# Kernel tuning notes

Measured on AMD Instinct MI355X. Metric: run time of the kernel, lower is better.

The kernel has to match this reference:

```python
import jax, jax.numpy as jnp
import numpy as np

B, H, W, C = 32, 64, 64, 256
NH, WS, SHIFT = 8, 8, 4
HD = C // NH
N = WS * WS           # tokens per window
NW = (H // WS) * (W // WS)
HID = 4 * C
EPS_LN = 1e-5
LOGIT_MAX = float(np.log(1.0 / 0.01))


def _rel_coords_table():
    ch = np.arange(-(WS - 1), WS, dtype=np.float32)
    t = np.stack(np.meshgrid(ch, ch, indexing='ij'), axis=-1)  # (2WS-1, 2WS-1, 2)
    t = t / (WS - 1) * 8.0
    t = np.sign(t) * np.log2(np.abs(t) + 1.0) / np.log2(8.0)
    return t.reshape(-1, 2)  # ((2WS-1)^2, 2)


def _rel_pos_index():
    coords = np.stack(np.meshgrid(np.arange(WS), np.arange(WS), indexing='ij'))
    cf = coords.reshape(2, -1)
    rel = (cf[:, :, None] - cf[:, None, :]).transpose(1, 2, 0).copy()
    rel[:, :, 0] += WS - 1
    rel[:, :, 1] += WS - 1
    rel[:, :, 0] *= 2 * WS - 1
    return rel.sum(-1)  # (N, N) int


def _attn_mask():
    img = np.zeros((H, W), np.float32)
    cnt = 0
    for hs in (slice(0, -WS), slice(-WS, -SHIFT), slice(-SHIFT, None)):
        for ws in (slice(0, -WS), slice(-WS, -SHIFT), slice(-SHIFT, None)):
            img[hs, ws] = cnt
            cnt += 1
    mw = img.reshape(H // WS, WS, W // WS, WS).transpose(0, 2, 1, 3).reshape(-1, N)
    diff = mw[:, None, :] - mw[:, :, None]
    return np.where(diff != 0, -100.0, 0.0).astype(np.float32)  # (NW, N, N)


_RCT = jnp.asarray(_rel_coords_table())
_RPI = jnp.asarray(_rel_pos_index())
_MASK = jnp.asarray(_attn_mask())


def _ln(x, g, b):
    mu = jnp.mean(x, axis=-1, keepdims=True)
    var = jnp.mean(jnp.square(x - mu), axis=-1, keepdims=True)
    return (x - mu) * jax.lax.rsqrt(var + EPS_LN) * g + b


def _l2n(x):
    return x / jnp.sqrt(jnp.maximum(jnp.sum(x * x, axis=-1, keepdims=True), 1e-12))


def setup_inputs() -> dict:
    key = jax.random.key(0)
    ks = jax.random.split(key, 16)
    s = 0.02
    return {
        'x': jax.random.normal(ks[0], (B, H * W, C), jnp.float32),
        'qkv_w': jax.random.normal(ks[1], (C, 3 * C), jnp.float32) * s,
        'q_bias': jnp.zeros((C,), jnp.float32),
        'v_bias': jnp.zeros((C,), jnp.float32),
        'logit_scale': jnp.full((NH, 1, 1), np.log(10.0), jnp.float32),
        'cpb_w1': jax.random.normal(ks[2], (2, 512), jnp.float32) * s,
        'cpb_b1': jnp.zeros((512,), jnp.float32),
        'cpb_w2': jax.random.normal(ks[3], (512, NH), jnp.float32) * s,
        'proj_w': jax.random.normal(ks[4], (C, C), jnp.float32) * s,
        'proj_b': jnp.zeros((C,), jnp.float32),
        'norm1_g': jnp.ones((C,), jnp.float32),
        'norm1_b': jnp.zeros((C,), jnp.float32),
        'fc1_w': jax.random.normal(ks[5], (C, HID), jnp.float32) * s,
        'fc1_b': jnp.zeros((HID,), jnp.float32),
        'fc2_w': jax.random.normal(ks[6], (HID, C), jnp.float32) * s,
        'fc2_b': jnp.zeros((C,), jnp.float32),
        'norm2_g': jnp.ones((C,), jnp.float32),
        'norm2_b': jnp.zeros((C,), jnp.float32),
    }


def reference(x, qkv_w, q_bias, v_bias, logit_scale, cpb_w1, cpb_b1, cpb_w2,
              proj_w, proj_b, norm1_g, norm1_b, fc1_w, fc1_b, fc2_w, fc2_b,
              norm2_g, norm2_b):
    shortcut = x
    xs = x.reshape(B, H, W, C)
    # cyclic shift
    xs = jnp.roll(xs, shift=(-SHIFT, -SHIFT), axis=(1, 2))
    # window partition -> (B*NW, N, C)
    xw = xs.reshape(B, H // WS, WS, W // WS, WS, C).transpose(0, 1, 3, 2, 4, 5)
    xw = xw.reshape(B * NW, N, C)

    # qkv projection (kernel without bias, then split q/v biases, k bias zero)
    qkv_bias = jnp.concatenate([q_bias, jnp.zeros_like(q_bias), v_bias], axis=0)
    qkv = xw @ qkv_w + qkv_bias
    qkv = qkv.reshape(B * NW, N, 3, NH, HD).transpose(2, 0, 3, 1, 4)
    q, k, v = qkv[0], qkv[1], qkv[2]  # (B*NW, NH, N, HD)

    # cosine attention
    attn = jnp.einsum('bhnd,bhmd->bhnm', _l2n(q), _l2n(k))
    scale = jnp.exp(jnp.minimum(logit_scale, LOGIT_MAX))  # (NH,1,1)
    attn = attn * scale

    # CPB-MLP relative position bias
    table = jax.nn.relu(_RCT @ cpb_w1 + cpb_b1) @ cpb_w2          # ((2WS-1)^2, NH)
    bias = table[_RPI]                                            # (N, N, NH)
    bias = 16.0 * jax.nn.sigmoid(bias.transpose(2, 0, 1))         # (NH, N, N)
    attn = attn + bias[None]

    # shifted-window mask
    attn = attn.reshape(B, NW, NH, N, N) + _MASK[None, :, None]
    attn = jax.nn.softmax(attn.reshape(B * NW, NH, N, N), axis=-1)

    out = jnp.einsum('bhnm,bhmd->bhnd', attn, v)
    out = out.transpose(0, 2, 1, 3).reshape(B * NW, N, C)
    out = out @ proj_w + proj_b

    # window reverse + reverse shift
    out = out.reshape(B, H // WS, W // WS, WS, WS, C).transpose(0, 1, 3, 2, 4, 5)
    out = out.reshape(B, H, W, C)
    out = jnp.roll(out, shift=(SHIFT, SHIFT), axis=(1, 2)).reshape(B, H * W, C)

    # SwinV2 post-norm residuals
    x = shortcut + _ln(out, norm1_g, norm1_b)
    h = jax.nn.gelu(x @ fc1_w + fc1_b, approximate=False) @ fc2_w + fc2_b
    x = x + _ln(h, norm2_g, norm2_b)
    return x
```

## Files before the change

kernel.cpp:

```cpp
#include <hip/hip_runtime.h>


#define TOKS 131072
#define LOGIT_MAX 4.60517018598809136804f

typedef __attribute__((ext_vector_type(8))) short short8;
typedef __attribute__((ext_vector_type(4))) float f32x4;

__device__ __forceinline__ float b2f(unsigned short s) {
    union { unsigned int u; float f; } x; x.u = ((unsigned int)s) << 16; return x.f;
}
__device__ __forceinline__ unsigned short f2b(float f) {
    union { float f; unsigned int u; } x; x.f = f;
    unsigned int r = x.u + 0x7fffu + ((x.u >> 16) & 1u);
    return (unsigned short)(r >> 16);
}

#define MFMA16(a, b, c) __builtin_amdgcn_mfma_f32_16x16x32_bf16((a), (b), (c), 0, 0, 0)

#define GLOAD_LDS16(g, l)                                                      \
    __builtin_amdgcn_global_load_lds(                                          \
        (const __attribute__((address_space(1))) void*)(g),                    \
        (__attribute__((address_space(3))) void*)(l), 16, 0, 0)


__global__ __launch_bounds__(256) void cvt_kernel(const float* __restrict__ in,
                                                  unsigned short* __restrict__ out, int n) {
    int i = (blockIdx.x * 256 + threadIdx.x) * 4;
    if (i >= n) return;
    float4 v = *(const float4*)(in + i);
    ushort4 o;
    o.x = f2b(v.x); o.y = f2b(v.y); o.z = f2b(v.z); o.w = f2b(v.w);
    *(ushort4*)(out + i) = o;
}

__global__ __launch_bounds__(256) void wt_kernel(const float* __restrict__ src,
                                                 unsigned short* __restrict__ dst,
                                                 int K, int N) {
    int idx = blockIdx.x * 256 + threadIdx.x;
    if (idx >= K * N) return;
    int n = idx / K, k = idx - n * K;
    dst[idx] = f2b(src[(size_t)k * N + n]);
}

__device__ __forceinline__ float cpb_coord(int d) {
    float t = (float)d * (8.0f / 7.0f);
    float a = log2f(fabsf(t) + 1.0f) * (1.0f / 3.0f);
    return t < 0.0f ? -a : a;
}

__global__ __launch_bounds__(256) void cpb_kernel(
    const float* __restrict__ w1, const float* __restrict__ b1, const float* __restrict__ w2,
    const float* __restrict__ qb, const float* __restrict__ vb,
    float* __restrict__ biasT, float* __restrict__ qkv_bias)
{
    __shared__ float tbl[225];
    int h = blockIdx.x, t = threadIdx.x;
    if (t < 225) {
        float r0 = cpb_coord(t / 15 - 7), r1 = cpb_coord(t % 15 - 7);
        float acc = 0.f;
        for (int j = 0; j < 512; ++j) {
            float hid = fmaxf(r0 * w1[j] + r1 * w1[512 + j] + b1[j], 0.f);
            acc += hid * w2[j * 8 + h];
        }
        tbl[t] = acc;
    }
    __syncthreads();
    for (int o = t; o < 4096; o += 256) {
        int i = o >> 6, j = o & 63;
        int idx = ((i >> 3) - (j >> 3) + 7) * 15 + ((i & 7) - (j & 7) + 7);
        biasT[h * 4096 + o] = 16.0f / (1.0f + __expf(-tbl[idx]));
    }
    if (h == 0)
        for (int n = t; n < 768; n += 256)
            qkv_bias[n] = n < 256 ? qb[n] : (n < 512 ? 0.f : vb[n - 512]);
}

template<int EPI, int GX>
__global__ __launch_bounds__(256) void gemm_bt(
    const unsigned short* __restrict__ A, const unsigned short* __restrict__ Bt,
    const float* __restrict__ bias, unsigned short* __restrict__ out,
    int M, int N, int K)
{
    __shared__ __align__(16) unsigned short sA[2][128 * 32];
    __shared__ __align__(16) unsigned short sB[2][128 * 32];
    const int tid = threadIdx.x;
    const int lane = tid & 63;
    const int wave = tid >> 6;
    const int wm = (wave >> 1) * 64, wn = (wave & 1) * 64;
    const int nwg = GX * (int)gridDim.y;
    int flat = (int)(blockIdx.y * GX + blockIdx.x);
    flat = (flat & 7) * (nwg >> 3) + (flat >> 3);
    const int bx = flat % GX;
    const int by = flat / GX;
    const int m0 = by * 128, n0 = bx * 128;
    const int l15 = lane & 15, lq = lane >> 4;
    const int r0 = tid >> 2, c0 = (tid & 3) << 3;

    const unsigned short* pA0 = A + (size_t)(m0 + r0) * K + c0;
    const unsigned short* pA1 = A + (size_t)(m0 + r0 + 64) * K + c0;
    const unsigned short* pB0 = Bt + (size_t)(n0 + r0) * K + c0;
    const unsigned short* pB1 = Bt + (size_t)(n0 + r0 + 64) * K + c0;

    auto stage = [&](int buf, int k0) {
        unsigned short* a = &sA[buf][wave * 512];
        unsigned short* b = &sB[buf][wave * 512];
        GLOAD_LDS16(pA0 + k0, a);
        GLOAD_LDS16(pA1 + k0, a + 2048);
        GLOAD_LDS16(pB0 + k0, b);
        GLOAD_LDS16(pB1 + k0, b + 2048);
    };

    f32x4 acc[4][4] = {};
    auto compute = [&](int buf) {
        short8 af[4], bw[4];
        #pragma unroll
        for (int t = 0; t < 4; ++t) {
            af[t] = *(const short8*)&sA[buf][(wm + t * 16 + l15) * 32 + lq * 8];
            bw[t] = *(const short8*)&sB[buf][(wn + t * 16 + l15) * 32 + lq * 8];
        }
        #pragma unroll
        for (int tm = 0; tm < 4; ++tm)
            #pragma unroll
            for (int tn = 0; tn < 4; ++tn)
                acc[tm][tn] = MFMA16(af[tm], bw[tn], acc[tm][tn]);
    };

    const int nt = K >> 5;
    stage(0, 0);
    for (int t = 0; t < nt - 1; ++t) {
        stage((t & 1) ^ 1, (t + 1) << 5);
        asm volatile("s_waitcnt vmcnt(4)" ::: "memory");
        __builtin_amdgcn_s_barrier();
        asm volatile("" ::: "memory");
        compute(t & 1);
        asm volatile("s_waitcnt lgkmcnt(0)" ::: "memory");
        __builtin_amdgcn_s_barrier();
    }
    asm volatile("s_waitcnt vmcnt(0)" ::: "memory");
    __builtin_amdgcn_s_barrier();
    asm volatile("" ::: "memory");
    compute((nt - 1) & 1);

    float bv[4];
    #pragma unroll
    for (int tn = 0; tn < 4; ++tn) bv[tn] = bias[n0 + wn + tn * 16 + l15];

    #pragma unroll
    for (int tm = 0; tm < 4; ++tm)
        #pragma unroll
        for (int tn = 0; tn < 4; ++tn)
            #pragma unroll
            for (int r = 0; r < 4; ++r) {
                int gm = m0 + wm + tm * 16 + lq * 4 + r;
                int gn = n0 + wn + tn * 16 + l15;
                float v = acc[tm][tn][r] + bv[tn];
                if constexpr (EPI == 2) {
                    float e = __expf(v * fmaf(-0.0713548162972754f, v * v,
                                              -1.5957691216057308f));
                    v = v * __builtin_amdgcn_rcpf(1.0f + e);
                }
                if constexpr (EPI == 1) {
                    int s = gn >> 8, hd = gn & 255;
                    out[((size_t)(s * 8 + (hd >> 5)) * TOKS + gm) * 32 + (hd & 31)] = f2b(v);
                } else {
                    out[(size_t)gm * N + gn] = f2b(v);
                }
            }
}

template<int MODE>
__global__ __launch_bounds__(256) void gemm_ln(
    const unsigned short* __restrict__ A, const unsigned short* __restrict__ Bt,
    const float* __restrict__ bias,
    const float* __restrict__ residf, const unsigned short* __restrict__ residb,
    const float* __restrict__ lng, const float* __restrict__ lnb,
    unsigned short* __restrict__ outb, float* __restrict__ outf, int K)
{
    __shared__ __align__(16) unsigned short sA[2][64 * 32];
    __shared__ __align__(16) unsigned short sB[2][256 * 32];
    const int tid = threadIdx.x;
    const int lane = tid & 63;
    const int wave = tid >> 6;
    const int wn = wave * 64;
    const int m0 = blockIdx.x * 64;
    const int l15 = lane & 15, lq = lane >> 4;
    const int r0 = tid >> 2, c0 = (tid & 3) << 3;

    const unsigned short* pA  = A + (size_t)(m0 + r0) * K + c0;
    const unsigned short* pB0 = Bt + (size_t)r0 * K + c0;
    const unsigned short* pB1 = pB0 + (size_t)64 * K;
    const unsigned short* pB2 = pB0 + (size_t)128 * K;
    const unsigned short* pB3 = pB0 + (size_t)192 * K;

    auto stage = [&](int buf, int k0) {
        unsigned short* a = &sA[buf][wave * 512];
        unsigned short* b = &sB[buf][wave * 512];
        GLOAD_LDS16(pA + k0, a);
        GLOAD_LDS16(pB0 + k0, b);
        GLOAD_LDS16(pB1 + k0, b + 2048);
        GLOAD_LDS16(pB2 + k0, b + 4096);
        GLOAD_LDS16(pB3 + k0, b + 6144);
    };

    f32x4 acc[4][4] = {};
    auto compute = [&](int buf) {
        short8 af[4], bw[4];
        #pragma unroll
        for (int t = 0; t < 4; ++t) {
            af[t] = *(const short8*)&sA[buf][(t * 16 + l15) * 32 + lq * 8];
            bw[t] = *(const short8*)&sB[buf][(wn + t * 16 + l15) * 32 + lq * 8];
        }
        #pragma unroll
        for (int tm = 0; tm < 4; ++tm)
            #pragma unroll
            for (int tn = 0; tn < 4; ++tn)
                acc[tm][tn] = MFMA16(af[tm], bw[tn], acc[tm][tn]);
    };

    const int nt = K >> 5;
    stage(0, 0);
    for (int t = 0; t < nt - 1; ++t) {
        stage((t & 1) ^ 1, (t + 1) << 5);
        asm volatile("s_waitcnt vmcnt(5)" ::: "memory");
        __builtin_amdgcn_s_barrier();
        asm volatile("" ::: "memory");
        compute(t & 1);
        asm volatile("s_waitcnt lgkmcnt(0)" ::: "memory");
        __builtin_amdgcn_s_barrier();
    }
    asm volatile("s_waitcnt vmcnt(0)" ::: "memory");
    __builtin_amdgcn_s_barrier();
    asm volatile("" ::: "memory");
    compute((nt - 1) & 1);
    asm volatile("s_waitcnt lgkmcnt(0)" ::: "memory");
    __builtin_amdgcn_s_barrier();

    float bv[4], gv[4], ev[4];
    #pragma unroll
    for (int tn = 0; tn < 4; ++tn) {
        int gn = wn + tn * 16 + l15;
        bv[tn] = bias[gn]; gv[tn] = lng[gn]; ev[tn] = lnb[gn];
    }

    float* sums = (float*)&sA[0][0];
    float* sqs  = (float*)&sA[0][0] + 256;
    #pragma unroll
    for (int tm = 0; tm < 4; ++tm)
        #pragma unroll
        for (int r = 0; r < 4; ++r) {
            int rl = tm * 16 + lq * 4 + r;
            float s = 0.f, q = 0.f;
            #pragma unroll
            for (int tn = 0; tn < 4; ++tn) {
                float v = acc[tm][tn][r] + bv[tn];
                s += v; q += v * v;
            }
            #pragma unroll
            for (int o = 1; o < 16; o <<= 1) { s += __shfl_xor(s, o); q += __shfl_xor(q, o); }
            if (l15 == 0) { sums[rl * 4 + wave] = s; sqs[rl * 4 + wave] = q; }
        }
    __syncthreads();

    #pragma unroll
    for (int tm = 0; tm < 4; ++tm)
        #pragma unroll
        for (int r = 0; r < 4; ++r) {
            int rl = tm * 16 + lq * 4 + r;
            float s = sums[rl * 4] + sums[rl * 4 + 1] + sums[rl * 4 + 2] + sums[rl * 4 + 3];
            float q = sqs[rl * 4] + sqs[rl * 4 + 1] + sqs[rl * 4 + 2] + sqs[rl * 4 + 3];
            float mu = s * (1.0f / 256.0f);
            float rs = rsqrtf(q * (1.0f / 256.0f) - mu * mu + 1e-5f);
            size_t rowo = (size_t)(m0 + rl) * 256;
            #pragma unroll
            for (int tn = 0; tn < 4; ++tn) {
                int gn = wn + tn * 16 + l15;
                float v = acc[tm][tn][r] + bv[tn];
                float nv = (v - mu) * rs * gv[tn] + ev[tn];
                if constexpr (MODE == 1)
                    outb[rowo + gn] = f2b(residf[rowo + gn] + nv);
                else
                    outf[rowo + gn] = b2f(residb[rowo + gn]) + nv;
            }
        }
}


__device__ __forceinline__ int regid(int wy, int wx, int t) {
    int y = wy * 8 + (t >> 3), x = wx * 8 + (t & 7);
    int ry = (y < 56) ? 0 : (y < 60 ? 1 : 2);
    int rx = (x < 56) ? 0 : (x < 60 ? 1 : 2);
    return ry * 3 + rx;
}

__device__ __forceinline__ void load_norm(const unsigned short* __restrict__ p,
                                          unsigned short* __restrict__ dst, int lane) {
    union U { uint4 u; unsigned short s[8]; };
    U ld[4];
    #pragma unroll
    for (int c = 0; c < 4; ++c) ld[c].u = *(const uint4*)(p + c * 8);
    float f[32]; float ss = 0.f;
    #pragma unroll
    for (int c = 0; c < 4; ++c)
        #pragma unroll
        for (int j = 0; j < 8; ++j) { float v = b2f(ld[c].s[j]); f[c * 8 + j] = v; ss += v * v; }
    float nrm = rsqrtf(fmaxf(ss, 1e-12f));
    #pragma unroll
    for (int c = 0; c < 4; ++c) {
        U st;
        #pragma unroll
        for (int j = 0; j < 8; ++j) st.s[j] = f2b(f[c * 8 + j] * nrm);
        *(uint4*)(dst + lane * 32 + c * 8) = st.u;
    }
}

__global__ __launch_bounds__(64) void attn_kernel(
    const unsigned short* __restrict__ qkv, const float* __restrict__ biasT,
    const float* __restrict__ ls, unsigned short* __restrict__ outb)
{
    __shared__ __align__(16) unsigned short sQ[64 * 32];
    __shared__ __align__(16) unsigned short sK[64 * 32];
    __shared__ __align__(16) unsigned short sV[64 * 32];
    __shared__ __align__(16) unsigned short sP[64 * 64];

    const int lane = threadIdx.x;
    const int h = blockIdx.x & 7;
    const int win = blockIdx.x >> 3;
    const int b = win >> 6;
    const int wy = (win >> 3) & 7, wx = win & 7;
    const int l15 = lane & 15, lq = lane >> 4;

    {
        int ty = lane >> 3, tx = lane & 7;
        int hh = (wy * 8 + ty + 4) & 63, ww = (wx * 8 + tx + 4) & 63;
        size_t tok = (size_t)b * 4096 + hh * 64 + ww;
        const size_t plane = (size_t)TOKS * 32;
        const unsigned short* qp = qkv + (size_t)h * plane + tok * 32;
        const unsigned short* kp = qkv + (size_t)(8 + h) * plane + tok * 32;
        const unsigned short* vp = qkv + (size_t)(16 + h) * plane + tok * 32;
        load_norm(qp, sQ, lane);
        load_norm(kp, sK, lane);
        #pragma unroll
        for (int c = 0; c < 4; ++c)
            *(uint4*)&sV[lane * 32 + c * 8] = *(const uint4*)(vp + c * 8);
    }
    __syncthreads();

    short8 aQ[4], bK[4];
    #pragma unroll
    for (int t = 0; t < 4; ++t) {
        aQ[t] = *(const short8*)&sQ[(t * 16 + l15) * 32 + lq * 8];
        bK[t] = *(const short8*)&sK[(t * 16 + l15) * 32 + lq * 8];
    }
    f32x4 acc[4][4] = {};
    #pragma unroll
    for (int tm = 0; tm < 4; ++tm)
        #pragma unroll
        for (int tn = 0; tn < 4; ++tn)
            acc[tm][tn] = MFMA16(aQ[tm], bK[tn], acc[tm][tn]);

    float scale = __expf(fminf(ls[h], LOGIT_MAX));

    #pragma unroll
    for (int tm = 0; tm < 4; ++tm)
        #pragma unroll
        for (int r = 0; r < 4; ++r) {
            int i = tm * 16 + lq * 4 + r;
            int ri = regid(wy, wx, i);
            float v[4];
            #pragma unroll
            for (int tn = 0; tn < 4; ++tn) {
                int j = tn * 16 + l15;
                float sc = acc[tm][tn][r] * scale + biasT[h * 4096 + i * 64 + j];
                if (ri != regid(wy, wx, j)) sc -= 100.f;
                v[tn] = sc;
            }
            float m = fmaxf(fmaxf(v[0], v[1]), fmaxf(v[2], v[3]));
            #pragma unroll
            for (int o = 1; o < 16; o <<= 1) m = fmaxf(m, __shfl_xor(m, o));
            float sum = 0.f;
            #pragma unroll
            for (int tn = 0; tn < 4; ++tn) { v[tn] = __expf(v[tn] - m); sum += v[tn]; }
            #pragma unroll
            for (int o = 1; o < 16; o <<= 1) sum += __shfl_xor(sum, o);
            float inv = 1.0f / sum;
            #pragma unroll
            for (int tn = 0; tn < 4; ++tn)
                sP[i * 64 + tn * 16 + l15] = f2b(v[tn] * inv);
        }
    __syncthreads();

    f32x4 accO[4][2] = {};
    #pragma unroll
    for (int ks = 0; ks < 2; ++ks) {
        short8 bV[2];
        #pragma unroll
        for (int tn = 0; tn < 2; ++tn)
            #pragma unroll
            for (int jj = 0; jj < 8; ++jj)
                bV[tn][jj] = (short)sV[(ks * 32 + lq * 8 + jj) * 32 + tn * 16 + l15];
        #pragma unroll
        for (int tm = 0; tm < 4; ++tm) {
            short8 aP = *(const short8*)&sP[(tm * 16 + l15) * 64 + ks * 32 + lq * 8];
            accO[tm][0] = MFMA16(aP, bV[0], accO[tm][0]);
            accO[tm][1] = MFMA16(aP, bV[1], accO[tm][1]);
        }
    }

    #pragma unroll
    for (int tm = 0; tm < 4; ++tm)
        #pragma unroll
        for (int r = 0; r < 4; ++r) {
            int i = tm * 16 + lq * 4 + r;
            int hh = (wy * 8 + (i >> 3) + 4) & 63, ww = (wx * 8 + (i & 7) + 4) & 63;
            size_t rowo = ((size_t)b * 4096 + hh * 64 + ww) * 256 + h * 32;
            outb[rowo + l15] = f2b(accO[tm][0][r]);
            outb[rowo + 16 + l15] = f2b(accO[tm][1][r]);
        }
}


extern "C" void kernel_launch(void* const* d_in, const int* in_sizes, int n_in,
                              void* d_out, int out_size, void* d_ws, size_t ws_size,
                              hipStream_t stream) {
    (void)in_sizes; (void)n_in; (void)out_size; (void)ws_size;
    const float* x      = (const float*)d_in[0];
    const float* qkv_w  = (const float*)d_in[1];
    const float* q_bias = (const float*)d_in[2];
    const float* v_bias = (const float*)d_in[3];
    const float* lscale = (const float*)d_in[4];
    const float* cpb_w1 = (const float*)d_in[5];
    const float* cpb_b1 = (const float*)d_in[6];
    const float* cpb_w2 = (const float*)d_in[7];
    const float* proj_w = (const float*)d_in[8];
    const float* proj_b = (const float*)d_in[9];
    const float* n1g    = (const float*)d_in[10];
    const float* n1b    = (const float*)d_in[11];
    const float* fc1_w  = (const float*)d_in[12];
    const float* fc1_b  = (const float*)d_in[13];
    const float* fc2_w  = (const float*)d_in[14];
    const float* fc2_b  = (const float*)d_in[15];
    const float* n2g    = (const float*)d_in[16];
    const float* n2b    = (const float*)d_in[17];

    char* ws = (char*)d_ws;
    unsigned short* R1 = (unsigned short*)(ws);
    unsigned short* R2 = (unsigned short*)(ws + 268435456);
    unsigned short* R3 = (unsigned short*)(ws + 335544320);
    unsigned short* qkv_wT = (unsigned short*)(ws + 402653184);
    unsigned short* proj_wT = (unsigned short*)(ws + 403046400);
    unsigned short* fc1_wT  = (unsigned short*)(ws + 403177472);
    unsigned short* fc2_wT  = (unsigned short*)(ws + 403701760);
    float* qkv_bias = (float*)(ws + 404226048);
    float* biasT    = (float*)(ws + 404229120);

    cvt_kernel<<<TOKS * 256 / 1024, 256, 0, stream>>>(x, R2, TOKS * 256);
    wt_kernel<<<(256 * 768 + 255) / 256, 256, 0, stream>>>(qkv_w, qkv_wT, 256, 768);
    wt_kernel<<<(256 * 256 + 255) / 256, 256, 0, stream>>>(proj_w, proj_wT, 256, 256);
    wt_kernel<<<(256 * 1024 + 255) / 256, 256, 0, stream>>>(fc1_w, fc1_wT, 256, 1024);
    wt_kernel<<<(1024 * 256 + 255) / 256, 256, 0, stream>>>(fc2_w, fc2_wT, 1024, 256);
    cpb_kernel<<<8, 256, 0, stream>>>(cpb_w1, cpb_b1, cpb_w2, q_bias, v_bias, biasT, qkv_bias);

    gemm_bt<1, 6><<<dim3(6, TOKS / 128), 256, 0, stream>>>(R2, qkv_wT, qkv_bias, R1, TOKS, 768, 256);
    attn_kernel<<<16384, 64, 0, stream>>>(R1, biasT, lscale, R2);
    gemm_ln<1><<<TOKS / 64, 256, 0, stream>>>(R2, proj_wT, proj_b, x, nullptr,
                                              n1g, n1b, R3, nullptr, 256);
    gemm_bt<2, 8><<<dim3(8, TOKS / 128), 256, 0, stream>>>(R3, fc1_wT, fc1_b, R1, TOKS, 1024, 256);
    gemm_ln<2><<<TOKS / 64, 256, 0, stream>>>(R1, fc2_wT, fc2_b, nullptr, R3,
                                              n2g, n2b, nullptr, (float*)d_out, 1024);
}
```

Before: 927.1 us.

## Make GEMMs persistent over four M-tiles with triple-buffered continuous K pipeline

Each GEMM workgroup now handles four consecutive M-tiles. The K-loop and the tile loop are flattened into one stream of stages, so global-to-LDS prefetch continues across tile boundaries and the epilogue runs in the middle of the stream. Buffering goes from double to triple with deeper vmcnt waits, and K becomes a compile-time template parameter. The aim is to hide load latency and amortize pipeline fill and drain, at the cost of more LDS, fewer workgroups (four times fewer blocks) and possible tail imbalance.

```diff
diff --git a/kernel.cpp b/kernel.cpp
--- a/kernel.cpp
+++ b/kernel.cpp
@@ -76,14 +76,16 @@
             qkv_bias[n] = n < 256 ? qb[n] : (n < 512 ? 0.f : vb[n - 512]);
 }
 
-template<int EPI, int GX>
+template<int EPI, int GX, int KT, int ML>
 __global__ __launch_bounds__(256) void gemm_bt(
     const unsigned short* __restrict__ A, const unsigned short* __restrict__ Bt,
-    const float* __restrict__ bias, unsigned short* __restrict__ out,
-    int M, int N, int K)
+    const float* __restrict__ bias, unsigned short* __restrict__ out, int N)
 {
-    __shared__ __align__(16) unsigned short sA[2][128 * 32];
-    __shared__ __align__(16) unsigned short sB[2][128 * 32];
+    constexpr int L2NT = (KT == 1024) ? 5 : 3;
+    constexpr int NT = 1 << L2NT;
+    constexpr int S = NT * ML;
+    __shared__ __align__(16) unsigned short sA[3][128 * 32];
+    __shared__ __align__(16) unsigned short sB[3][128 * 32];
     const int tid = threadIdx.x;
     const int lane = tid & 63;
     const int wave = tid >> 6;
@@ -93,20 +95,23 @@
     flat = (flat & 7) * (nwg >> 3) + (flat >> 3);
     const int bx = flat % GX;
     const int by = flat / GX;
-    const int m0 = by * 128, n0 = bx * 128;
+    const int mb0 = by * (128 * ML), n0 = bx * 128;
     const int l15 = lane & 15, lq = lane >> 4;
     const int r0 = tid >> 2, c0 = (tid & 3) << 3;
 
-    const unsigned short* pA0 = A + (size_t)(m0 + r0) * K + c0;
-    const unsigned short* pA1 = A + (size_t)(m0 + r0 + 64) * K + c0;
-    const unsigned short* pB0 = Bt + (size_t)(n0 + r0) * K + c0;
-    const unsigned short* pB1 = Bt + (size_t)(n0 + r0 + 64) * K + c0;
-
-    auto stage = [&](int buf, int k0) {
+    const unsigned short* pA0 = A + (size_t)(mb0 + r0) * KT + c0;
+    const unsigned short* pA1 = pA0 + (size_t)64 * KT;
+    const unsigned short* pB0 = Bt + (size_t)(n0 + r0) * KT + c0;
+    const unsigned short* pB1 = pB0 + (size_t)64 * KT;
+
+    auto stage = [&](int buf, int s) {
+        int mt = s >> L2NT;
+        int k0 = (s & (NT - 1)) << 5;
+        size_t aoff = (size_t)mt * (128 * KT) + k0;
         unsigned short* a = &sA[buf][wave * 512];
         unsigned short* b = &sB[buf][wave * 512];
-        GLOAD_LDS16(pA0 + k0, a);
-        GLOAD_LDS16(pA1 + k0, a + 2048);
+        GLOAD_LDS16(pA0 + aoff, a);
+        GLOAD_LDS16(pA1 + aoff, a + 2048);
         GLOAD_LDS16(pB0 + k0, b);
         GLOAD_LDS16(pB1 + k0, b + 2048);
     };
@@ -126,77 +131,96 @@
                 acc[tm][tn] = MFMA16(af[tm], bw[tn], acc[tm][tn]);
     };
 
-    const int nt = K >> 5;
+    float bv[4];
+    #pragma unroll
+    for (int tn = 0; tn < 4; ++tn) bv[tn] = bias[n0 + wn + tn * 16 + l15];
+
     stage(0, 0);
-    for (int t = 0; t < nt - 1; ++t) {
-        stage((t & 1) ^ 1, (t + 1) << 5);
-        asm volatile("s_waitcnt vmcnt(4)" ::: "memory");
+    stage(1, 1);
+    int cb = 0, sb = 2;
+    #pragma unroll 1
+    for (int s = 0; s < S; ++s) {
+        if (s + 2 < S) {
+            stage(sb, s + 2);
+            sb = (sb == 2) ? 0 : sb + 1;
+            asm volatile("s_waitcnt vmcnt(8)" ::: "memory");
+        } else if (s + 1 < S) {
+            asm volatile("s_waitcnt vmcnt(4)" ::: "memory");
+        } else {
+            asm volatile("s_waitcnt vmcnt(0)" ::: "memory");
+        }
         __builtin_amdgcn_s_barrier();
         asm volatile("" ::: "memory");
-        compute(t & 1);
+        compute(cb);
         asm volatile("s_waitcnt lgkmcnt(0)" ::: "memory");
         __builtin_amdgcn_s_barrier();
-    }
-    asm volatile("s_waitcnt vmcnt(0)" ::: "memory");
-    __builtin_amdgcn_s_barrier();
-    asm volatile("" ::: "memory");
-    compute((nt - 1) & 1);
-
-    float bv[4];
-    #pragma unroll
-    for (int tn = 0; tn < 4; ++tn) bv[tn] = bias[n0 + wn + tn * 16 + l15];
-
-    #pragma unroll
-    for (int tm = 0; tm < 4; ++tm)
-        #pragma unroll
-        for (int tn = 0; tn < 4; ++tn)
-            #pragma unroll
-            for (int r = 0; r < 4; ++r) {
-                int gm = m0 + wm + tm * 16 + lq * 4 + r;
-                int gn = n0 + wn + tn * 16 + l15;
-                float v = acc[tm][tn][r] + bv[tn];
-                if constexpr (EPI == 2) {
-                    float e = __expf(v * fmaf(-0.0713548162972754f, v * v,
-                                              -1.5957691216057308f));
-                    v = v * __builtin_amdgcn_rcpf(1.0f + e);
+        cb = (cb == 2) ? 0 : cb + 1;
+
+        if ((s & (NT - 1)) == NT - 1) {
+            const int m0 = mb0 + (s >> L2NT) * 128;
+            #pragma unroll
+            for (int tm = 0; tm < 4; ++tm)
+                #pragma unroll
+                for (int tn = 0; tn < 4; ++tn) {
+                    #pragma unroll
+                    for (int r = 0; r < 4; ++r) {
+                        int gm = m0 + wm + tm * 16 + lq * 4 + r;
+                        int gn = n0 + wn + tn * 16 + l15;
+                        float v = acc[tm][tn][r] + bv[tn];
+                        if constexpr (EPI == 2) {
+                            float e = __expf(v * fmaf(-0.0713548162972754f, v * v,
+                                                      -1.5957691216057308f));
+                            v = v * __builtin_amdgcn_rcpf(1.0f + e);
+                        }
+                        if constexpr (EPI == 1) {
+                            int sp = gn >> 8, hd = gn & 255;
+                            out[((size_t)(sp * 8 + (hd >> 5)) * TOKS + gm) * 32 + (hd & 31)] = f2b(v);
+                        } else {
+                            out[(size_t)gm * N + gn] = f2b(v);
+                        }
+                    }
+                    acc[tm][tn] = (f32x4){0.f, 0.f, 0.f, 0.f};
                 }
-                if constexpr (EPI == 1) {
-                    int s = gn >> 8, hd = gn & 255;
-                    out[((size_t)(s * 8 + (hd >> 5)) * TOKS + gm) * 32 + (hd & 31)] = f2b(v);
-                } else {
-                    out[(size_t)gm * N + gn] = f2b(v);
-                }
-            }
-}
-
-template<int MODE>
+        }
+    }
+}
+
+template<int MODE, int KT, int ML>
 __global__ __launch_bounds__(256) void gemm_ln(
     const unsigned short* __restrict__ A, const unsigned short* __restrict__ Bt,
     const float* __restrict__ bias,
     const float* __restrict__ residf, const unsigned short* __restrict__ residb,
     const float* __restrict__ lng, const float* __restrict__ lnb,
-    unsigned short* __restrict__ outb, float* __restrict__ outf, int K)
+    unsigned short* __restrict__ outb, float* __restrict__ outf)
 {
-    __shared__ __align__(16) unsigned short sA[2][64 * 32];
-    __shared__ __align__(16) unsigned short sB[2][256 * 32];
+    constexpr int L2NT = (KT == 1024) ? 5 : 3;
+    constexpr int NT = 1 << L2NT;
+    constexpr int S = NT * ML;
+    __shared__ __align__(16) unsigned short sA[3][64 * 32];
+    __shared__ __align__(16) unsigned short sB[3][256 * 32];
+    __shared__ float sums[256];
+    __shared__ float sqs[256];
     const int tid = threadIdx.x;
     const int lane = tid & 63;
     const int wave = tid >> 6;
     const int wn = wave * 64;
-    const int m0 = blockIdx.x * 64;
+    const int mb0 = blockIdx.x * (64 * ML);
     const int l15 = lane & 15, lq = lane >> 4;
     const int r0 = tid >> 2, c0 = (tid & 3) << 3;
 
-    const unsigned short* pA  = A + (size_t)(m0 + r0) * K + c0;
-    const unsigned short* pB0 = Bt + (size_t)r0 * K + c0;
-    const unsigned short* pB1 = pB0 + (size_t)64 * K;
-    const unsigned short* pB2 = pB0 + (size_t)128 * K;
-    const unsigned short* pB3 = pB0 + (size_t)192 * K;
-
-    auto stage = [&](int buf, int k0) {
+    const unsigned short* pA  = A + (size_t)(mb0 + r0) * KT + c0;
+    const unsigned short* pB0 = Bt + (size_t)r0 * KT + c0;
+    const unsigned short* pB1 = pB0 + (size_t)64 * KT;
+    const unsigned short* pB2 = pB0 + (size_t)128 * KT;
+    const unsigned short* pB3 = pB0 + (size_t)192 * KT;
+
+    auto stage = [&](int buf, int s) {
+        int mt = s >> L2NT;
+        int k0 = (s & (NT - 1)) << 5;
+        size_t aoff = (size_t)mt * (64 * KT) + k0;
         unsigned short* a = &sA[buf][wave * 512];
         unsigned short* b = &sB[buf][wave * 512];
-        GLOAD_LDS16(pA + k0, a);
+        GLOAD_LDS16(pA + aoff, a);
         GLOAD_LDS16(pB0 + k0, b);
         GLOAD_LDS16(pB1 + k0, b + 2048);
         GLOAD_LDS16(pB2 + k0, b + 4096);
@@ -218,24 +242,6 @@
                 acc[tm][tn] = MFMA16(af[tm], bw[tn], acc[tm][tn]);
     };
 
-    const int nt = K >> 5;
-    stage(0, 0);
-    for (int t = 0; t < nt - 1; ++t) {
-        stage((t & 1) ^ 1, (t + 1) << 5);
-        asm volatile("s_waitcnt vmcnt(5)" ::: "memory");
-        __builtin_amdgcn_s_barrier();
-        asm volatile("" ::: "memory");
-        compute(t & 1);
-        asm volatile("s_waitcnt lgkmcnt(0)" ::: "memory");
-        __builtin_amdgcn_s_barrier();
-    }
-    asm volatile("s_waitcnt vmcnt(0)" ::: "memory");
-    __builtin_amdgcn_s_barrier();
-    asm volatile("" ::: "memory");
-    compute((nt - 1) & 1);
-    asm volatile("s_waitcnt lgkmcnt(0)" ::: "memory");
-    __builtin_amdgcn_s_barrier();
-
     float bv[4], gv[4], ev[4];
     #pragma unroll
     for (int tn = 0; tn < 4; ++tn) {
@@ -243,46 +249,76 @@
         bv[tn] = bias[gn]; gv[tn] = lng[gn]; ev[tn] = lnb[gn];
     }
 
-    float* sums = (float*)&sA[0][0];
-    float* sqs  = (float*)&sA[0][0] + 256;
-    #pragma unroll
-    for (int tm = 0; tm < 4; ++tm)
-        #pragma unroll
-        for (int r = 0; r < 4; ++r) {
-            int rl = tm * 16 + lq * 4 + r;
-            float s = 0.f, q = 0.f;
-            #pragma unroll
-            for (int tn = 0; tn < 4; ++tn) {
-                float v = acc[tm][tn][r] + bv[tn];
-                s += v; q += v * v;
-            }
-            #pragma unroll
-            for (int o = 1; o < 16; o <<= 1) { s += __shfl_xor(s, o); q += __shfl_xor(q, o); }
-            if (l15 == 0) { sums[rl * 4 + wave] = s; sqs[rl * 4 + wave] = q; }
-        }
-    __syncthreads();
-
-    #pragma unroll
-    for (int tm = 0; tm < 4; ++tm)
-        #pragma unroll
-        for (int r = 0; r < 4; ++r) {
-            int rl = tm * 16 + lq * 4 + r;
-            float s = sums[rl * 4] + sums[rl * 4 + 1] + sums[rl * 4 + 2] + sums[rl * 4 + 3];
-            float q = sqs[rl * 4] + sqs[rl * 4 + 1] + sqs[rl * 4 + 2] + sqs[rl * 4 + 3];
-            float mu = s * (1.0f / 256.0f);
-            float rs = rsqrtf(q * (1.0f / 256.0f) - mu * mu + 1e-5f);
-            size_t rowo = (size_t)(m0 + rl) * 256;
-            #pragma unroll
-            for (int tn = 0; tn < 4; ++tn) {
-                int gn = wn + tn * 16 + l15;
-                float v = acc[tm][tn][r] + bv[tn];
-                float nv = (v - mu) * rs * gv[tn] + ev[tn];
-                if constexpr (MODE == 1)
-                    outb[rowo + gn] = f2b(residf[rowo + gn] + nv);
-                else
-                    outf[rowo + gn] = b2f(residb[rowo + gn]) + nv;
-            }
-        }
+    stage(0, 0);
+    stage(1, 1);
+    int cb = 0, sb = 2;
+    #pragma unroll 1
+    for (int s = 0; s < S; ++s) {
+        if (s + 2 < S) {
+            stage(sb, s + 2);
+            sb = (sb == 2) ? 0 : sb + 1;
+            asm volatile("s_waitcnt vmcnt(10)" ::: "memory");
+        } else if (s + 1 < S) {
+            asm volatile("s_waitcnt vmcnt(5)" ::: "memory");
+        } else {
+            asm volatile("s_waitcnt vmcnt(0)" ::: "memory");
+        }
+        __builtin_amdgcn_s_barrier();
+        asm volatile("" ::: "memory");
+        compute(cb);
+        asm volatile("s_waitcnt lgkmcnt(0)" ::: "memory");
+        __builtin_amdgcn_s_barrier();
+        cb = (cb == 2) ? 0 : cb + 1;
+
+        if ((s & (NT - 1)) == NT - 1) {
+            const int m0 = mb0 + (s >> L2NT) * 64;
+            #pragma unroll
+            for (int tm = 0; tm < 4; ++tm)
+                #pragma unroll
+                for (int r = 0; r < 4; ++r) {
+                    int rl = tm * 16 + lq * 4 + r;
+                    float ss = 0.f, qq = 0.f;
+                    #pragma unroll
+                    for (int tn = 0; tn < 4; ++tn) {
+                        float v = acc[tm][tn][r] + bv[tn];
+                        ss += v; qq += v * v;
+                    }
+                    #pragma unroll
+                    for (int o = 1; o < 16; o <<= 1) {
+                        ss += __shfl_xor(ss, o); qq += __shfl_xor(qq, o);
+                    }
+                    if (l15 == 0) { sums[rl * 4 + wave] = ss; sqs[rl * 4 + wave] = qq; }
+                }
+            asm volatile("s_waitcnt lgkmcnt(0)" ::: "memory");
+            __builtin_amdgcn_s_barrier();
+            #pragma unroll
+            for (int tm = 0; tm < 4; ++tm)
+                #pragma unroll
+                for (int r = 0; r < 4; ++r) {
+                    int rl = tm * 16 + lq * 4 + r;
+                    float ss = sums[rl * 4] + sums[rl * 4 + 1] + sums[rl * 4 + 2] + sums[rl * 4 + 3];
+                    float qq = sqs[rl * 4] + sqs[rl * 4 + 1] + sqs[rl * 4 + 2] + sqs[rl * 4 + 3];
+                    float mu = ss * (1.0f / 256.0f);
+                    float rs = rsqrtf(qq * (1.0f / 256.0f) - mu * mu + 1e-5f);
+                    size_t rowo = (size_t)(m0 + rl) * 256;
+                    #pragma unroll
+                    for (int tn = 0; tn < 4; ++tn) {
+                        int gn = wn + tn * 16 + l15;
+                        float v = acc[tm][tn][r] + bv[tn];
+                        float nv = (v - mu) * rs * gv[tn] + ev[tn];
+                        if constexpr (MODE == 1)
+                            outb[rowo + gn] = f2b(residf[rowo + gn] + nv);
+                        else
+                            outf[rowo + gn] = b2f(residb[rowo + gn]) + nv;
+                    }
+                }
+            #pragma unroll
+            for (int tm = 0; tm < 4; ++tm)
+                #pragma unroll
+                for (int tn = 0; tn < 4; ++tn)
+                    acc[tm][tn] = (f32x4){0.f, 0.f, 0.f, 0.f};
+        }
+    }
 }
 
 
@@ -461,11 +497,11 @@
     wt_kernel<<<(1024 * 256 + 255) / 256, 256, 0, stream>>>(fc2_w, fc2_wT, 1024, 256);
     cpb_kernel<<<8, 256, 0, stream>>>(cpb_w1, cpb_b1, cpb_w2, q_bias, v_bias, biasT, qkv_bias);
 
-    gemm_bt<1, 6><<<dim3(6, TOKS / 128), 256, 0, stream>>>(R2, qkv_wT, qkv_bias, R1, TOKS, 768, 256);
+    gemm_bt<1, 6, 256, 4><<<dim3(6, TOKS / 512), 256, 0, stream>>>(R2, qkv_wT, qkv_bias, R1, 768);
     attn_kernel<<<16384, 64, 0, stream>>>(R1, biasT, lscale, R2);
-    gemm_ln<1><<<TOKS / 64, 256, 0, stream>>>(R2, proj_wT, proj_b, x, nullptr,
-                                              n1g, n1b, R3, nullptr, 256);
-    gemm_bt<2, 8><<<dim3(8, TOKS / 128), 256, 0, stream>>>(R3, fc1_wT, fc1_b, R1, TOKS, 1024, 256);
-    gemm_ln<2><<<TOKS / 64, 256, 0, stream>>>(R1, fc2_wT, fc2_b, nullptr, R3,
-                                              n2g, n2b, nullptr, (float*)d_out, 1024);
-}
+    gemm_ln<1, 256, 4><<<TOKS / 256, 256, 0, stream>>>(R2, proj_wT, proj_b, x, nullptr,
+                                                       n1g, n1b, R3, nullptr);
+    gemm_bt<2, 8, 256, 4><<<dim3(8, TOKS / 512), 256, 0, stream>>>(R3, fc1_wT, fc1_b, R1, 1024);
+    gemm_ln<2, 1024, 4><<<TOKS / 256, 256, 0, stream>>>(R1, fc2_wT, fc2_b, nullptr, R3,
+                                                        n2g, n2b, nullptr, (float*)d_out);
+}
```

Result: slower. 1.213 ms (+30.9%).

## Fuse fc1, GELU, fc2 and LayerNorm into a single MLP kernel

Applied to the files above, without the earlier changes.

Replaces the separate fc1 GEMM (with GELU epilogue) and the fc2 GEMM+LayerNorm kernel with one kernel per 64-row tile. The kernel keeps the hidden activation chunk in a swizzled LDS buffer and streams the weights through it, so the 1024-wide hidden tensor is never written to or read from global memory. The price is higher LDS usage per block (about 80KB), which lowers occupancy, and each block re-reads both full weight matrices. The GELU epilogue code in gemm_bt is dropped because that path is no longer used.

```diff
diff --git a/kernel.cpp b/kernel.cpp
--- a/kernel.cpp
+++ b/kernel.cpp
@@ -22,6 +22,11 @@
     __builtin_amdgcn_global_load_lds(                                          \
         (const __attribute__((address_space(1))) void*)(g),                    \
         (__attribute__((address_space(3))) void*)(l), 16, 0, 0)
+
+#define S_VMCNT(N) asm volatile("s_waitcnt vmcnt(" #N ")" ::: "memory")
+#define S_LGKM0()  asm volatile("s_waitcnt lgkmcnt(0)" ::: "memory")
+#define S_BAR()    __builtin_amdgcn_s_barrier()
+#define S_FENCE()  asm volatile("" ::: "memory")
 
 
 __global__ __launch_bounds__(256) void cvt_kernel(const float* __restrict__ in,
@@ -130,16 +135,14 @@
     stage(0, 0);
     for (int t = 0; t < nt - 1; ++t) {
         stage((t & 1) ^ 1, (t + 1) << 5);
-        asm volatile("s_waitcnt vmcnt(4)" ::: "memory");
-        __builtin_amdgcn_s_barrier();
-        asm volatile("" ::: "memory");
+        S_VMCNT(4);
+        S_BAR(); S_FENCE();
         compute(t & 1);
-        asm volatile("s_waitcnt lgkmcnt(0)" ::: "memory");
-        __builtin_amdgcn_s_barrier();
-    }
-    asm volatile("s_waitcnt vmcnt(0)" ::: "memory");
-    __builtin_amdgcn_s_barrier();
-    asm volatile("" ::: "memory");
+        S_LGKM0();
+        S_BAR();
+    }
+    S_VMCNT(0);
+    S_BAR(); S_FENCE();
     compute((nt - 1) & 1);
 
     float bv[4];
@@ -155,11 +158,6 @@
                 int gm = m0 + wm + tm * 16 + lq * 4 + r;
                 int gn = n0 + wn + tn * 16 + l15;
                 float v = acc[tm][tn][r] + bv[tn];
-                if constexpr (EPI == 2) {
-                    float e = __expf(v * fmaf(-0.0713548162972754f, v * v,
-                                              -1.5957691216057308f));
-                    v = v * __builtin_amdgcn_rcpf(1.0f + e);
-                }
                 if constexpr (EPI == 1) {
                     int s = gn >> 8, hd = gn & 255;
                     out[((size_t)(s * 8 + (hd >> 5)) * TOKS + gm) * 32 + (hd & 31)] = f2b(v);
@@ -222,19 +220,17 @@
     stage(0, 0);
     for (int t = 0; t < nt - 1; ++t) {
         stage((t & 1) ^ 1, (t + 1) << 5);
-        asm volatile("s_waitcnt vmcnt(5)" ::: "memory");
-        __builtin_amdgcn_s_barrier();
-        asm volatile("" ::: "memory");
+        S_VMCNT(5);
+        S_BAR(); S_FENCE();
         compute(t & 1);
-        asm volatile("s_waitcnt lgkmcnt(0)" ::: "memory");
-        __builtin_amdgcn_s_barrier();
-    }
-    asm volatile("s_waitcnt vmcnt(0)" ::: "memory");
-    __builtin_amdgcn_s_barrier();
-    asm volatile("" ::: "memory");
+        S_LGKM0();
+        S_BAR();
+    }
+    S_VMCNT(0);
+    S_BAR(); S_FENCE();
     compute((nt - 1) & 1);
-    asm volatile("s_waitcnt lgkmcnt(0)" ::: "memory");
-    __builtin_amdgcn_s_barrier();
+    S_LGKM0();
+    S_BAR();
 
     float bv[4], gv[4], ev[4];
     #pragma unroll
@@ -281,6 +277,171 @@
                     outb[rowo + gn] = f2b(residf[rowo + gn] + nv);
                 else
                     outf[rowo + gn] = b2f(residb[rowo + gn]) + nv;
+            }
+        }
+}
+
+__global__ __launch_bounds__(256) void mlp_kernel(
+    const unsigned short* __restrict__ x1,
+    const unsigned short* __restrict__ w1t,
+    const float* __restrict__ b1,
+    const unsigned short* __restrict__ w2t,
+    const float* __restrict__ b2,
+    const float* __restrict__ lng, const float* __restrict__ lnb,
+    float* __restrict__ outf)
+{
+    __shared__ __align__(16) unsigned short sW[2][256 * 32];
+    __shared__ __align__(16) unsigned short sA[2][64 * 32];
+    __shared__ __align__(16) unsigned short sH[64 * 256];
+    __shared__ float sums[256], sqs[256];
+
+    const int tid = threadIdx.x;
+    const int lane = tid & 63;
+    const int wave = tid >> 6;
+    const int wn = wave * 64;
+    const int m0 = blockIdx.x * 64;
+    const int l15 = lane & 15, lq = lane >> 4;
+    const int r0 = tid >> 2, c0 = (tid & 3) << 3;
+
+    const unsigned short* pX  = x1 + (size_t)(m0 + r0) * 256 + c0;
+    const unsigned short* pW1 = w1t + (size_t)r0 * 256 + c0;
+    const unsigned short* pW2 = w2t + (size_t)r0 * 1024 + c0;
+
+    float b1v[4][4], b2v[4], gv[4], ev[4];
+    #pragma unroll
+    for (int c = 0; c < 4; ++c)
+        #pragma unroll
+        for (int tn = 0; tn < 4; ++tn)
+            b1v[c][tn] = b1[c * 256 + wn + tn * 16 + l15];
+    #pragma unroll
+    for (int tn = 0; tn < 4; ++tn) {
+        int gn = wn + tn * 16 + l15;
+        b2v[tn] = b2[gn]; gv[tn] = lng[gn]; ev[tn] = lnb[gn];
+    }
+
+    auto stage1 = [&](int buf, int c, int t) {
+        int kk = t * 32;
+        GLOAD_LDS16(pX + kk, &sA[buf][wave * 512]);
+        const unsigned short* w = pW1 + (size_t)(c * 256) * 256 + kk;
+        #pragma unroll
+        for (int q = 0; q < 4; ++q)
+            GLOAD_LDS16(w + (size_t)(q * 64) * 256, &sW[buf][q * 2048 + wave * 512]);
+    };
+    auto stage2 = [&](int buf, int c, int t) {
+        int kk = c * 256 + t * 32;
+        #pragma unroll
+        for (int q = 0; q < 4; ++q)
+            GLOAD_LDS16(pW2 + (size_t)(q * 64) * 1024 + kk, &sW[buf][q * 2048 + wave * 512]);
+    };
+
+    f32x4 acc1[4][4] = {};
+    f32x4 acc2[4][4] = {};
+
+    auto comp1 = [&](int buf) {
+        short8 af[4], bw[4];
+        #pragma unroll
+        for (int t = 0; t < 4; ++t) {
+            af[t] = *(const short8*)&sA[buf][(t * 16 + l15) * 32 + lq * 8];
+            bw[t] = *(const short8*)&sW[buf][(wn + t * 16 + l15) * 32 + lq * 8];
+        }
+        #pragma unroll
+        for (int tm = 0; tm < 4; ++tm)
+            #pragma unroll
+            for (int tn = 0; tn < 4; ++tn)
+                acc1[tm][tn] = MFMA16(af[tm], bw[tn], acc1[tm][tn]);
+    };
+    auto comp2 = [&](int buf, int t) {
+        short8 af[4], bw[4];
+        #pragma unroll
+        for (int tt = 0; tt < 4; ++tt) {
+            unsigned rb = tt * 16 + l15;
+            unsigned byte = (rb * 512u + (unsigned)(t * 64 + lq * 16)) ^ ((rb & 7u) << 4);
+            af[tt] = *(const short8*)((const char*)sH + byte);
+            bw[tt] = *(const short8*)&sW[buf][(wn + tt * 16 + l15) * 32 + lq * 8];
+        }
+        #pragma unroll
+        for (int tm = 0; tm < 4; ++tm)
+            #pragma unroll
+            for (int tn = 0; tn < 4; ++tn)
+                acc2[tm][tn] = MFMA16(af[tm], bw[tn], acc2[tm][tn]);
+    };
+
+    stage1(0, 0, 0);
+    #pragma unroll
+    for (int c = 0; c < 4; ++c) {
+        #pragma unroll
+        for (int t = 0; t < 8; ++t) {
+            if (t < 7) { stage1((t + 1) & 1, c, t + 1); S_VMCNT(5); }
+            else       { stage2(0, c, 0);               S_VMCNT(4); }
+            S_BAR(); S_FENCE();
+            comp1(t & 1);
+            S_LGKM0();
+            S_BAR();
+        }
+        #pragma unroll
+        for (int tm = 0; tm < 4; ++tm)
+            #pragma unroll
+            for (int tn = 0; tn < 4; ++tn) {
+                #pragma unroll
+                for (int r = 0; r < 4; ++r) {
+                    unsigned row = tm * 16 + lq * 4 + r;
+                    unsigned col = wn + tn * 16 + l15;
+                    float v = acc1[tm][tn][r] + b1v[c][tn];
+                    float e = __expf(v * fmaf(-0.0713548162972754f, v * v,
+                                              -1.5957691216057308f));
+                    v = v * __builtin_amdgcn_rcpf(1.0f + e);
+                    unsigned byte = (row * 512u + col * 2u) ^ ((row & 7u) << 4);
+                    *(unsigned short*)((char*)sH + byte) = f2b(v);
+                }
+                acc1[tm][tn] = (f32x4){0.f, 0.f, 0.f, 0.f};
+            }
+        S_LGKM0();
+        S_BAR();
+        #pragma unroll
+        for (int t = 0; t < 8; ++t) {
+            if (t < 7)      { stage2((t + 1) & 1, c, t + 1); S_VMCNT(4); }
+            else if (c < 3) { stage1(0, c + 1, 0);           S_VMCNT(5); }
+            else            { S_VMCNT(0); }
+            S_BAR(); S_FENCE();
+            comp2(t & 1, t);
+            S_LGKM0();
+            S_BAR();
+        }
+    }
+
+    #pragma unroll
+    for (int tm = 0; tm < 4; ++tm)
+        #pragma unroll
+        for (int r = 0; r < 4; ++r) {
+            int rl = tm * 16 + lq * 4 + r;
+            float ss = 0.f, qq = 0.f;
+            #pragma unroll
+            for (int tn = 0; tn < 4; ++tn) {
+                float v = acc2[tm][tn][r] + b2v[tn];
+                ss += v; qq += v * v;
+            }
+            #pragma unroll
+            for (int o = 1; o < 16; o <<= 1) { ss += __shfl_xor(ss, o); qq += __shfl_xor(qq, o); }
+            if (l15 == 0) { sums[rl * 4 + wave] = ss; sqs[rl * 4 + wave] = qq; }
+        }
+    S_LGKM0();
+    S_BAR();
+    #pragma unroll
+    for (int tm = 0; tm < 4; ++tm)
+        #pragma unroll
+        for (int r = 0; r < 4; ++r) {
+            int rl = tm * 16 + lq * 4 + r;
+            float ss = sums[rl * 4] + sums[rl * 4 + 1] + sums[rl * 4 + 2] + sums[rl * 4 + 3];
+            float qq = sqs[rl * 4] + sqs[rl * 4 + 1] + sqs[rl * 4 + 2] + sqs[rl * 4 + 3];
+            float mu = ss * (1.0f / 256.0f);
+            float rs = rsqrtf(qq * (1.0f / 256.0f) - mu * mu + 1e-5f);
+            size_t rowo = (size_t)(m0 + rl) * 256;
+            #pragma unroll
+            for (int tn = 0; tn < 4; ++tn) {
+                int gn = wn + tn * 16 + l15;
+                float v = acc2[tm][tn][r] + b2v[tn];
+                float nv = (v - mu) * rs * gv[tn] + ev[tn];
+                outf[rowo + gn] = b2f(x1[rowo + gn]) + nv;
             }
         }
 }
@@ -465,7 +626,6 @@
     attn_kernel<<<16384, 64, 0, stream>>>(R1, biasT, lscale, R2);
     gemm_ln<1><<<TOKS / 64, 256, 0, stream>>>(R2, proj_wT, proj_b, x, nullptr,
                                               n1g, n1b, R3, nullptr, 256);
-    gemm_bt<2, 8><<<dim3(8, TOKS / 128), 256, 0, stream>>>(R3, fc1_wT, fc1_b, R1, TOKS, 1024, 256);
-    gemm_ln<2><<<TOKS / 64, 256, 0, stream>>>(R1, fc2_wT, fc2_b, nullptr, R3,
-                                              n2g, n2b, nullptr, (float*)d_out, 1024);
-}
+    mlp_kernel<<<TOKS / 64, 256, 0, stream>>>(R3, fc1_wT, fc1_b, fc2_wT, fc2_b,
+                                              n2g, n2b, (float*)d_out);
+}
```

Result: slower. 954.2 us (+2.9%).

## Load Q/K directly into MFMA registers and store V transposed with XOR swizzle

Applied to the files above, without the earlier changes.

The attention kernel now loads Q and K straight from global memory into the MFMA operand layout and does the L2 normalisation in registers, using cross-lane shuffles to sum the squares. This removes the sQ/sK shared buffers and the first barrier. V is written to shared memory transposed with an XOR swizzle, so the PV operand becomes one vector LDS read instead of eight scalar reads. The Q/K global loads are less coalesced in exchange, and the first barrier is gone, so the ordering between the sVT writes and the later reads now rests on the remaining barrier.

```diff
diff --git a/kernel.cpp b/kernel.cpp
--- a/kernel.cpp
+++ b/kernel.cpp
@@ -293,34 +293,11 @@
     return ry * 3 + rx;
 }
 
-__device__ __forceinline__ void load_norm(const unsigned short* __restrict__ p,
-                                          unsigned short* __restrict__ dst, int lane) {
-    union U { uint4 u; unsigned short s[8]; };
-    U ld[4];
-    #pragma unroll
-    for (int c = 0; c < 4; ++c) ld[c].u = *(const uint4*)(p + c * 8);
-    float f[32]; float ss = 0.f;
-    #pragma unroll
-    for (int c = 0; c < 4; ++c)
-        #pragma unroll
-        for (int j = 0; j < 8; ++j) { float v = b2f(ld[c].s[j]); f[c * 8 + j] = v; ss += v * v; }
-    float nrm = rsqrtf(fmaxf(ss, 1e-12f));
-    #pragma unroll
-    for (int c = 0; c < 4; ++c) {
-        U st;
-        #pragma unroll
-        for (int j = 0; j < 8; ++j) st.s[j] = f2b(f[c * 8 + j] * nrm);
-        *(uint4*)(dst + lane * 32 + c * 8) = st.u;
-    }
-}
-
 __global__ __launch_bounds__(64) void attn_kernel(
     const unsigned short* __restrict__ qkv, const float* __restrict__ biasT,
     const float* __restrict__ ls, unsigned short* __restrict__ outb)
 {
-    __shared__ __align__(16) unsigned short sQ[64 * 32];
-    __shared__ __align__(16) unsigned short sK[64 * 32];
-    __shared__ __align__(16) unsigned short sV[64 * 32];
+    __shared__ __align__(16) unsigned short sVT[32 * 64];
     __shared__ __align__(16) unsigned short sP[64 * 64];
 
     const int lane = threadIdx.x;
@@ -329,29 +306,54 @@
     const int b = win >> 6;
     const int wy = (win >> 3) & 7, wx = win & 7;
     const int l15 = lane & 15, lq = lane >> 4;
-
+    const size_t plane = (size_t)TOKS * 32;
+    const size_t base = (size_t)b * 4096;
+
+    union U { uint4 u; unsigned short s[8]; };
+
+    U vld[4];
     {
-        int ty = lane >> 3, tx = lane & 7;
-        int hh = (wy * 8 + ty + 4) & 63, ww = (wx * 8 + tx + 4) & 63;
-        size_t tok = (size_t)b * 4096 + hh * 64 + ww;
-        const size_t plane = (size_t)TOKS * 32;
-        const unsigned short* qp = qkv + (size_t)h * plane + tok * 32;
-        const unsigned short* kp = qkv + (size_t)(8 + h) * plane + tok * 32;
-        const unsigned short* vp = qkv + (size_t)(16 + h) * plane + tok * 32;
-        load_norm(qp, sQ, lane);
-        load_norm(kp, sK, lane);
-        #pragma unroll
-        for (int c = 0; c < 4; ++c)
-            *(uint4*)&sV[lane * 32 + c * 8] = *(const uint4*)(vp + c * 8);
-    }
-    __syncthreads();
+        int hh = (wy * 8 + (lane >> 3) + 4) & 63, ww = (wx * 8 + (lane & 7) + 4) & 63;
+        const unsigned short* vp = qkv + (size_t)(16 + h) * plane + (base + hh * 64 + ww) * 32;
+        #pragma unroll
+        for (int c = 0; c < 4; ++c) vld[c].u = *(const uint4*)(vp + c * 8);
+    }
+
+    U qld[4], kld[4];
+    #pragma unroll
+    for (int t = 0; t < 4; ++t) {
+        int i = t * 16 + l15;
+        int hh = (wy * 8 + (i >> 3) + 4) & 63, ww = (wx * 8 + (i & 7) + 4) & 63;
+        size_t tok = base + hh * 64 + ww;
+        qld[t].u = *(const uint4*)(qkv + (size_t)h * plane + tok * 32 + lq * 8);
+        kld[t].u = *(const uint4*)(qkv + (size_t)(8 + h) * plane + tok * 32 + lq * 8);
+    }
+
+    #pragma unroll
+    for (int c = 0; c < 4; ++c)
+        #pragma unroll
+        for (int j = 0; j < 8; ++j)
+            sVT[(c * 8 + j) * 64 + (lane ^ (j << 3))] = vld[c].s[j];
 
     short8 aQ[4], bK[4];
     #pragma unroll
     for (int t = 0; t < 4; ++t) {
-        aQ[t] = *(const short8*)&sQ[(t * 16 + l15) * 32 + lq * 8];
-        bK[t] = *(const short8*)&sK[(t * 16 + l15) * 32 + lq * 8];
-    }
+        float qf[8], kf[8]; float qs = 0.f, kss = 0.f;
+        #pragma unroll
+        for (int j = 0; j < 8; ++j) {
+            qf[j] = b2f(qld[t].s[j]); qs += qf[j] * qf[j];
+            kf[j] = b2f(kld[t].s[j]); kss += kf[j] * kf[j];
+        }
+        qs += __shfl_xor(qs, 16);  qs += __shfl_xor(qs, 32);
+        kss += __shfl_xor(kss, 16); kss += __shfl_xor(kss, 32);
+        float qn = rsqrtf(fmaxf(qs, 1e-12f)), kn = rsqrtf(fmaxf(kss, 1e-12f));
+        #pragma unroll
+        for (int j = 0; j < 8; ++j) {
+            aQ[t][j] = (short)f2b(qf[j] * qn);
+            bK[t][j] = (short)f2b(kf[j] * kn);
+        }
+    }
+
     f32x4 acc[4][4] = {};
     #pragma unroll
     for (int tm = 0; tm < 4; ++tm)
@@ -395,10 +397,11 @@
     for (int ks = 0; ks < 2; ++ks) {
         short8 bV[2];
         #pragma unroll
-        for (int tn = 0; tn < 2; ++tn)
-            #pragma unroll
-            for (int jj = 0; jj < 8; ++jj)
-                bV[tn][jj] = (short)sV[(ks * 32 + lq * 8 + jj) * 32 + tn * 16 + l15];
+        for (int tn = 0; tn < 2; ++tn) {
+            int d = tn * 16 + l15;
+            int t8 = (ks * 32 + lq * 8) ^ ((l15 & 7) << 3);
+            bV[tn] = *(const short8*)&sVT[d * 64 + t8];
+        }
         #pragma unroll
         for (int tm = 0; tm < 4; ++tm) {
             short8 aP = *(const short8*)&sP[(tm * 16 + l15) * 64 + ks * 32 + lq * 8];
@@ -413,7 +416,7 @@
         for (int r = 0; r < 4; ++r) {
             int i = tm * 16 + lq * 4 + r;
             int hh = (wy * 8 + (i >> 3) + 4) & 63, ww = (wx * 8 + (i & 7) + 4) & 63;
-            size_t rowo = ((size_t)b * 4096 + hh * 64 + ww) * 256 + h * 32;
+            size_t rowo = (base + hh * 64 + ww) * 256 + h * 32;
             outb[rowo + l15] = f2b(accO[tm][0][r]);
             outb[rowo + 16 + l15] = f2b(accO[tm][1][r]);
         }
```

Result: no change. 923.5 us (-0.4%).
